# Performance work log

Measured on AMD Instinct MI355X. Metric: run time of the kernel, lower is better.

## Reference

```python
import jax, jax.numpy as jnp
import numpy as np

NH = 1024
NV = 31
LAYERS = 2
BS = 64
SEQ = 512
EPS = 1e-5


def _gru_layer(x_seq, h0, Wih, Whh, bih, bhh):
    """x_seq: [B,S,in], h0: [B,nh]. PyTorch GRU gate math. Returns [B,S,nh], h_last."""
    # Precompute input-side gates for all timesteps: [B,S,3nh]
    xg = jnp.einsum('bsi,gi->bsg', x_seq, Wih) + bih
    xg = jnp.swapaxes(xg, 0, 1)  # [S,B,3nh] for scan over time

    def step(h, xg_t):
        hg = h @ Whh.T + bhh  # [B,3nh]
        xr, xz, xn = jnp.split(xg_t, 3, axis=-1)
        hr, hz, hn = jnp.split(hg, 3, axis=-1)
        r = jax.nn.sigmoid(xr + hr)
        z = jax.nn.sigmoid(xz + hz)
        n = jnp.tanh(xn + r * hn)
        h_new = (1.0 - z) * n + z * h
        return h_new, h_new

    h_last, ys = jax.lax.scan(step, h0, xg)
    return jnp.swapaxes(ys, 0, 1), h_last  # [B,S,nh]


def setup_inputs() -> dict:
    key = jax.random.key(0)
    ks = jax.random.split(key, 16)
    s = 0.02
    inp = {
        'x': jax.random.randint(ks[0], (BS, SEQ), 0, NV),
        'h0': jnp.zeros((LAYERS, BS, NH), jnp.float32),
        'emb': jax.random.normal(ks[1], (NV, NH), jnp.float32) * s,
        'Wih0': jax.random.normal(ks[2], (3 * NH, NH), jnp.float32) * s,
        'Whh0': jax.random.normal(ks[3], (3 * NH, NH), jnp.float32) * s,
        'bih0': jnp.zeros((3 * NH,), jnp.float32),
        'bhh0': jnp.zeros((3 * NH,), jnp.float32),
        'Wih1': jax.random.normal(ks[4], (3 * NH, NH), jnp.float32) * s,
        'Whh1': jax.random.normal(ks[5], (3 * NH, NH), jnp.float32) * s,
        'bih1': jnp.zeros((3 * NH,), jnp.float32),
        'bhh1': jnp.zeros((3 * NH,), jnp.float32),
        'gamma': jnp.ones((NH,), jnp.float32),
        'beta': jnp.zeros((NH,), jnp.float32),
        'Wout': jax.random.normal(ks[6], (NV, NH), jnp.float32) * s,
        'bout': jnp.zeros((NV,), jnp.float32),
    }
    return inp


def reference(x, h0, emb, Wih0, Whh0, bih0, bhh0, Wih1, Whh1, bih1, bhh1,
              gamma, beta, Wout, bout):
    e = emb[x]  # [B,S,nh] embedding lookup
    y0, _ = _gru_layer(e, h0[0], Wih0, Whh0, bih0, bhh0)
    y1, _ = _gru_layer(y0, h0[1], Wih1, Whh1, bih1, bhh1)
    # BatchNorm1dFlat: flatten (B*S, nh), batch-statistics BN, reshape back
    flat = y1.reshape(-1, NH)
    mu = flat.mean(axis=0)
    var = flat.var(axis=0)  # biased, as in BN training
    bn = (y1 - mu) * jax.lax.rsqrt(var + EPS) * gamma + beta
    return bn @ Wout.T + bout  # [B,S,nv]
```

## Files before the change

### kernel.cpp

```cpp
#include <hip/hip_runtime.h>
#include <cstddef>
#include <stdint.h>

#define NHID 1024
#define NVOC 31
#define NB   64
#define NSEQ 512
#define NWRK 192
#define NGRID 256
#define NTHR 512
#define EPSV 1e-5f
#define RS2  36
#define SL   (NB*NHID)
#define XG_SLOTS 16

typedef __attribute__((ext_vector_type(8))) short short8;
typedef __attribute__((ext_vector_type(4))) float float4v;

#define OFF_F0  0
#define OFF_F1  4096
#define OFF_F2  8192
#define OFF_FIN 12288
#define CNT_BYTES 12352

#define M_OFF_Y0  12544
#define M_OFF_Y1  (M_OFF_Y0 + 513ull*SL*2)
#define M_OFF_H1I (M_OFF_Y1 + 512ull*SL*2)
#define M_OFF_T0  (M_OFF_H1I + (unsigned long long)SL*2)
#define M_OFF_ST  (M_OFF_T0 + 31ull*3*NHID*4)
#define M_OFF_XG  (M_OFF_ST + 16384ull)

#define LDS_BYTES 65024

__device__ __forceinline__ unsigned short f2bf(float f){
  unsigned u = __builtin_bit_cast(unsigned, f);
  u += 0x7fffu + ((u >> 16) & 1u);
  return (unsigned short)(u >> 16);
}
__device__ __forceinline__ float bf2f(unsigned short h){
  unsigned u = ((unsigned)h) << 16;
  return __builtin_bit_cast(float, u);
}
__device__ __forceinline__ float sigm(float x){ return 1.f/(1.f + __expf(-x)); }
__device__ __forceinline__ float tanh_f(float x){ return 1.f - 2.f/(__expf(2.f*x) + 1.f); }

__device__ __forceinline__ void burn(float& d){
#pragma unroll
  for (int i=0;i<16;++i)
    asm volatile("v_fmac_f32 %0, %1, %2" : "+v"(d) : "v"(d), "v"(d));
}

__device__ __forceinline__ void setflag(unsigned* f, unsigned v){
  __hip_atomic_store(f, v, __ATOMIC_RELAXED, __HIP_MEMORY_SCOPE_AGENT);
}
__device__ __forceinline__ void waitflags4(const unsigned* f, int base4, int target, int lane, float& d){
  const unsigned* p = f + (size_t)(base4 + (lane & 3))*16;
  for(;;){
    int v = (int)__hip_atomic_load(p, __ATOMIC_RELAXED, __HIP_MEMORY_SCOPE_AGENT);
    if (__all(v >= target)) break;
    burn(d);
  }
  asm volatile("" ::: "memory");
}
__device__ __forceinline__ void waitflag1(const unsigned* f, int idx, int target, float& d){
  const unsigned* p = f + (size_t)idx*16;
  while ((int)__hip_atomic_load(p, __ATOMIC_RELAXED, __HIP_MEMORY_SCOPE_AGENT) < target)
    burn(d);
  asm volatile("" ::: "memory");
}
__device__ __forceinline__ void waitflag1_slow(const unsigned* f, int idx, int target, float& d){
  const unsigned* p = f + (size_t)idx*16;
  while ((int)__hip_atomic_load(p, __ATOMIC_RELAXED, __HIP_MEMORY_SCOPE_AGENT) < target){
    burn(d); burn(d); burn(d); burn(d);
  }
  asm volatile("" ::: "memory");
}
__device__ __forceinline__ void sig(unsigned* c){
  __hip_atomic_fetch_add(c, 1u, __ATOMIC_RELAXED, __HIP_MEMORY_SCOPE_AGENT);
}
__device__ __forceinline__ void waitc(unsigned* c, unsigned v, float& d){
  while (__hip_atomic_load(c, __ATOMIC_RELAXED, __HIP_MEMORY_SCOPE_AGENT) < v)
    burn(d);
}

__device__ __forceinline__ void stc16(void* p, short8 v){
  asm volatile("global_store_dwordx4 %0, %1, off sc1"
               :: "v"((unsigned long long)(uintptr_t)p), "v"(v) : "memory");
}
__device__ __forceinline__ void stc4(void* p, float v){
  asm volatile("global_store_dword %0, %1, off sc1"
               :: "v"((unsigned long long)(uintptr_t)p), "v"(v) : "memory");
}
__device__ __forceinline__ void stc4u(void* p, unsigned v){
  asm volatile("global_store_dword %0, %1, off sc1"
               :: "v"((unsigned long long)(uintptr_t)p), "v"(v) : "memory");
}
__device__ __forceinline__ void drain_vm(){
  asm volatile("s_waitcnt vmcnt(0)" ::: "memory");
}

__device__ __forceinline__ void load_bfrags6(const float* W, int ch0,
                                             short8 (&bfr)[6][4], int lane, int wid)
{
  const int l15 = lane & 15, q = lane >> 4;
#pragma unroll
  for (int nt=0; nt<6; ++nt){
    int grow = (nt>>1)*NHID + ch0 + (nt&1)*16 + l15;
    const float* wp0 = W + (size_t)grow*NHID + wid*128 + q*8;
#pragma unroll
    for (int kt=0; kt<4; ++kt){
      const float* wp = wp0 + kt*32;
      short8 fr;
#pragma unroll
      for (int j=0;j<8;++j) fr[j] = (short)f2bf(wp[j]);
      bfr[nt][kt] = fr;
    }
  }
}
__device__ __forceinline__ void load_a2(const unsigned short* slab, int b0,
                                        short8 (&f)[2][4], int lane, int wid)
{
#pragma unroll
  for (int mt=0;mt<2;++mt){
    const short8* p = (const short8*)(slab + (size_t)(b0 + mt*16 + (lane&15))*NHID
                                      + wid*128 + (lane>>4)*8);
#pragma unroll
    for (int kt=0;kt<4;++kt) f[mt][kt] = p[kt*4];
  }
}
__device__ __forceinline__ void gemm2d(const short8 (&fA)[2][4],
                                       const short8 (&bfr)[6][4],
                                       float* red, int lane, int wid)
{
  const int l15 = lane & 15, q = lane >> 4;
  float4v acc[2][6];
#pragma unroll
  for (int mt=0; mt<2; ++mt)
#pragma unroll
    for (int nt=0; nt<6; ++nt) acc[mt][nt] = (float4v){0.f,0.f,0.f,0.f};
#pragma unroll
  for (int kt=0; kt<4; ++kt){
#pragma unroll
    for (int nt=0; nt<6; ++nt){
      acc[0][nt] = __builtin_amdgcn_mfma_f32_16x16x32_bf16(fA[0][kt], bfr[nt][kt], acc[0][nt],0,0,0);
      acc[1][nt] = __builtin_amdgcn_mfma_f32_16x16x32_bf16(fA[1][kt], bfr[nt][kt], acc[1][nt],0,0,0);
    }
  }
  if (wid >= 4){
#pragma unroll
    for (int mt=0; mt<2; ++mt)
#pragma unroll
      for (int nt=0; nt<6; ++nt){
        int n = nt*16 + l15, row = mt*16 + q*4;
        *(float4v*)(red + ((wid-4)*96 + n)*RS2 + row) = acc[mt][nt];
      }
  }
  __syncthreads();
  if (wid < 4){
#pragma unroll
    for (int mt=0; mt<2; ++mt)
#pragma unroll
      for (int nt=0; nt<6; ++nt){
        int n = nt*16 + l15, row = mt*16 + q*4;
        float4v* p = (float4v*)(red + (wid*96 + n)*RS2 + row);
        float4v v = *p;
        *p = v + acc[mt][nt];
      }
  }
  __syncthreads();
}

__global__ __launch_bounds__(NTHR, 2) void mgru_fused(
    const int*   __restrict__ x,    const float* __restrict__ h0,
    const float* __restrict__ emb,
    const float* __restrict__ Wih0, const float* __restrict__ Whh0,
    const float* __restrict__ bih0, const float* __restrict__ bhh0,
    const float* __restrict__ Wih1, const float* __restrict__ Whh1,
    const float* __restrict__ bih1, const float* __restrict__ bhh1,
    const float* __restrict__ gamma, const float* __restrict__ beta,
    const float* __restrict__ Wout, const float* __restrict__ bout,
    float* __restrict__ out, char* ws)
{
  __shared__ __align__(16) char smem[LDS_BYTES];
  float* red = (float*)smem;

  unsigned* f0  = (unsigned*)(ws + OFF_F0);
  unsigned* f1  = (unsigned*)(ws + OFF_F1);
  unsigned* f2  = (unsigned*)(ws + OFF_F2);
  unsigned* fin = (unsigned*)(ws + OFF_FIN);
  unsigned short* y0b   = (unsigned short*)(ws + M_OFF_Y0);
  unsigned short* y1    = (unsigned short*)(ws + M_OFF_Y1);
  unsigned short* h1i   = (unsigned short*)(ws + M_OFF_H1I);
  float*          T0    = (float*)(ws + M_OFF_T0);
  float*          stats = (float*)(ws + M_OFF_ST);
  float*          xgring= (float*)(ws + M_OFF_XG);

  const int tid  = threadIdx.x;
  const int lane = tid & 63;
  const int wid  = tid >> 6;
  const int wg   = blockIdx.x;
  const int l15 = lane & 15, q = lane >> 4;
  float dummy = (float)tid * 1e-30f + 1.0f;

  if (wg >= NWRK){
    for(;;){
      for (int i=0;i<64;++i) burn(dummy);
      unsigned v = __hip_atomic_load(fin, __ATOMIC_RELAXED, __HIP_MEMORY_SCOPE_AGENT);
      if (v >= (unsigned)NWRK) break;
    }
    if (tid == 0) __threadfence();
    __syncthreads();
    if (dummy == 1234.5678f) ((volatile float*)smem)[0] = dummy;
    goto epilogue;
  }

  {
    if (tid == 0) __threadfence();
    __syncthreads();

    const int role = (wg < 64) ? 0 : (wg < 128 ? 1 : 2);

    const int gm = tid >> 4;
    const int gc = (tid & 15) * 2;

    if (role == 0){
      const int rw = wg, bg = rw >> 5, cg = rw & 31;
      const int b0 = bg*32, ch0 = cg*32;
      const int fidx = bg*32 + cg;
      const int gbat = b0 + gm;
      short8 bfr0[6][4];
      float hprev[2];
      float br[2], bz[2], bn[2];

      {
        unsigned pk2 = 0;
#pragma unroll
        for (int j=0;j<2;++j){
          int ch = ch0 + gc + j;
          hprev[j] = h0[(size_t)gbat*NHID + ch];
          br[j] = bhh0[ch]; bz[j] = bhh0[NHID + ch]; bn[j] = bhh0[2*NHID + ch];
          pk2 |= (unsigned)f2bf(hprev[j]) << (16*j);
        }
        stc4u(y0b + (size_t)gbat*NHID + ch0 + gc, pk2);
        drain_vm();
      }
      __syncthreads();
      if (tid == 0) setflag(f0 + (size_t)fidx*16, 1u);

      for (int e = tid; e < NVOC*96; e += NTHR){
        int v = e / 96, n = e - v*96;
        int gate = n >> 5, c32 = n & 31;
        int grow = gate*NHID + ch0 + c32;
        const float4v* e4 = (const float4v*)(emb  + (size_t)v*NHID);
        const float4v* w4 = (const float4v*)(Wih0 + (size_t)grow*NHID);
        float acc = 0.f;
        for (int k=0;k<NHID/4;++k){
          float4v a = e4[k], bb = w4[k];
          acc += a[0]*bb[0] + a[1]*bb[1] + a[2]*bb[2] + a[3]*bb[3];
        }
        T0[(size_t)v*3*NHID + grow] = acc + bih0[grow];
      }
      load_bfrags6(Whh0, ch0, bfr0, lane, wid);
      __syncthreads();

      for (int t = 0; t < NSEQ; ++t){
        waitflags4(f0, bg*32 + wid*4, t+1, lane, dummy);
        short8 fA[2][4];
        load_a2(y0b + (size_t)t*SL, b0, fA, lane, wid);
        gemm2d(fA, bfr0, red, lane, wid);
        {
          int tok = x[(size_t)gbat*NSEQ + t];
          const float* tp = T0 + (size_t)tok*3*NHID;
          unsigned pk2 = 0;
#pragma unroll
          for (int j=0;j<2;++j){
            int c32 = gc + j, ch = ch0 + c32;
            float hr = br[j], hz = bz[j], hn = bn[j];
#pragma unroll
            for (int w=0;w<4;++w){
              hr += red[(w*96 +      c32)*RS2 + gm];
              hz += red[(w*96 + 32 + c32)*RS2 + gm];
              hn += red[(w*96 + 64 + c32)*RS2 + gm];
            }
            float r = sigm(tp[ch] + hr);
            float z = sigm(tp[NHID + ch] + hz);
            float n = tanh_f(tp[2*NHID + ch] + r*hn);
            float hnv = (1.f - z)*n + z*hprev[j];
            hprev[j] = hnv;
            pk2 |= (unsigned)f2bf(hnv) << (16*j);
          }
          stc4u(y0b + (size_t)(t+1)*SL + (size_t)gbat*NHID + ch0 + gc, pk2);
          drain_vm();
        }
        __syncthreads();
        if (tid == 0) setflag(f0 + (size_t)fidx*16, (unsigned)(t+2));
      }

    } else if (role == 1){
      const int rw = wg - 64, bg = rw >> 5, cg = rw & 31;
      const int b0 = bg*32, ch0 = cg*32;
      const int fidx = bg*32 + cg;
      short8 wf[6][4];
      load_bfrags6(Wih1, ch0, wf, lane, wid);
      __syncthreads();

      for (int t = 0; t < NSEQ; ++t){
        if ((t & 3) == 0 && t >= 16)
          waitflag1_slow(f2, fidx, t-11, dummy);
        waitflags4(f0, bg*32 + wid*4, t+2, lane, dummy);
        short8 fB[2][4];
        load_a2(y0b + (size_t)(t+1)*SL, b0, fB, lane, wid);
        gemm2d(fB, wf, red, lane, wid);
        float* xgw = xgring + ((size_t)(t & (XG_SLOTS-1))*64 + (size_t)fidx)*3072;
#pragma unroll
        for (int i=0;i<6;++i){
          int idx = tid + i*512;
          int n = idx >> 5, m = idx & 31;
          float v = bih1[(n>>5)*NHID + ch0 + (n&31)];
          v += red[(      n)*RS2 + m];
          v += red[( 96 + n)*RS2 + m];
          v += red[(192 + n)*RS2 + m];
          v += red[(288 + n)*RS2 + m];
          stc4(xgw + idx, v);
        }
        drain_vm();
        __syncthreads();
        if (tid == 0) setflag(f1 + (size_t)fidx*16, (unsigned)(t+2));
      }

    } else {
      const int rw = wg - 128, bg = rw >> 5, cg = rw & 31;
      const int b0 = bg*32, ch0 = cg*32;
      const int fidx = bg*32 + cg;
      const int gbat = b0 + gm;
      short8 bfrH[6][4];
      float hprev[2];
      float bhr[2], bhz[2], bhn[2];
      float s1[2] = {0,0}, s2[2] = {0,0};

      {
        unsigned pk2 = 0;
#pragma unroll
        for (int j=0;j<2;++j){
          int ch = ch0 + gc + j;
          hprev[j] = h0[(size_t)NB*NHID + (size_t)gbat*NHID + ch];
          bhr[j] = bhh1[ch]; bhz[j] = bhh1[NHID + ch]; bhn[j] = bhh1[2*NHID + ch];
          pk2 |= (unsigned)f2bf(hprev[j]) << (16*j);
        }
        stc4u(h1i + (size_t)gbat*NHID + ch0 + gc, pk2);
        drain_vm();
      }
      __syncthreads();
      if (tid == 0) setflag(f2 + (size_t)fidx*16, 1u);

      load_bfrags6(Whh1, ch0, bfrH, lane, wid);
      __syncthreads();

      for (int t = 0; t < NSEQ; ++t){
        waitflags4(f2, bg*32 + wid*4, t+1, lane, dummy);
        const unsigned short* hsrc = (t == 0) ? h1i : (y1 + (size_t)(t-1)*SL);
        short8 fH[2][4];
        load_a2(hsrc, b0, fH, lane, wid);
        gemm2d(fH, bfrH, red, lane, wid);
        {
          float hrv[2], hzv[2], hnv_[2];
#pragma unroll
          for (int j=0;j<2;++j){
            int c32 = gc + j;
            float hr = bhr[j], hz = bhz[j], hn = bhn[j];
#pragma unroll
            for (int w=0;w<4;++w){
              hr += red[(w*96 +      c32)*RS2 + gm];
              hz += red[(w*96 + 32 + c32)*RS2 + gm];
              hn += red[(w*96 + 64 + c32)*RS2 + gm];
            }
            hrv[j] = hr; hzv[j] = hz; hnv_[j] = hn;
          }
          waitflag1(f1, fidx, t+2, dummy);
          const float* xgt = xgring + ((size_t)(t & (XG_SLOTS-1))*64 + (size_t)fidx)*3072;
          unsigned pk2 = 0;
#pragma unroll
          for (int j=0;j<2;++j){
            int c32 = gc + j;
            float xr = __hip_atomic_load(xgt + (size_t)(     c32)*32 + gm, __ATOMIC_RELAXED, __HIP_MEMORY_SCOPE_AGENT);
            float xz = __hip_atomic_load(xgt + (size_t)(32 + c32)*32 + gm, __ATOMIC_RELAXED, __HIP_MEMORY_SCOPE_AGENT);
            float xn = __hip_atomic_load(xgt + (size_t)(64 + c32)*32 + gm, __ATOMIC_RELAXED, __HIP_MEMORY_SCOPE_AGENT);
            float r  = sigm(xr + hrv[j]);
            float z  = sigm(xz + hzv[j]);
            float nn = tanh_f(xn + r*hnv_[j]);
            float hnew = (1.f - z)*nn + z*hprev[j];
            hprev[j] = hnew;
            unsigned short hb = f2bf(hnew);
            pk2 |= (unsigned)hb << (16*j);
            float hq = bf2f(hb);
            s1[j] += hq; s2[j] += hq*hq;
          }
          stc4u(y1 + (size_t)t*SL + (size_t)gbat*NHID + ch0 + gc, pk2);
          drain_vm();
        }
        __syncthreads();
        if (tid == 0) setflag(f2 + (size_t)fidx*16, (unsigned)(t+2));
      }

      {
        float* sb = (float*)smem;
        __syncthreads();
#pragma unroll
        for (int j=0;j<2;++j) sb[(gc + j)*32 + gm] = s1[j];
        __syncthreads();
        if (tid < 32){
          float a = 0.f;
          for (int i=0;i<32;++i) a += sb[tid*32 + i];
          stats[(size_t)bg*2048 + ch0 + tid] = a;
        }
        __syncthreads();
#pragma unroll
        for (int j=0;j<2;++j) sb[(gc + j)*32 + gm] = s2[j];
        __syncthreads();
        if (tid < 32){
          float a = 0.f;
          for (int i=0;i<32;++i) a += sb[tid*32 + i];
          stats[(size_t)bg*2048 + 1024 + ch0 + tid] = a;
        }
      }
    }

    __syncthreads();
    if (tid == 0){
      __threadfence();
      sig(fin);
      waitc(fin, NWRK, dummy);
      __threadfence();
    }
    __syncthreads();
    if (dummy == 1234.5678f) ((volatile float*)smem)[0] = dummy;
  }

epilogue:
  {
    const float inv_n = 1.f/32768.f;

    float* bpart    = (float*)smem;
    float* bprime_l = (float*)(smem + 2048);
    {
      int v = tid >> 4, k0 = tid & 15;
      float partial = 0.f;
      if (v < NVOC){
        for (int k = k0; k < NHID; k += 16){
          float s1k = stats[k] + stats[2048 + k];
          float s2k = stats[1024 + k] + stats[3072 + k];
          float mu  = s1k*inv_n;
          float var = s2k*inv_n - mu*mu;
          float sc  = gamma[k]*rsqrtf(var + EPSV);
          partial += (beta[k] - mu*sc) * Wout[(size_t)v*NHID + k];
        }
      }
      bpart[tid] = partial;
    }
    __syncthreads();
    if (tid < 32){
      float bpv = 0.f;
      for (int j=0;j<16;++j) bpv += bpart[tid*16 + j];
      bprime_l[tid] = (tid < NVOC) ? (bpv + bout[tid]) : 0.f;
    }
    __syncthreads();
    float bp_a = bprime_l[l15];
    float bp_b = (l15 < 15) ? bprime_l[16 + l15] : 0.f;
    __syncthreads();

    unsigned short* wsc = (unsigned short*)smem;
    for (int e = tid; e < NVOC*1032; e += NTHR){
      int v = e / 1032, k = e - v*1032;
      float val = 0.f;
      if (k < NHID){
        float s1k = stats[k] + stats[2048 + k];
        float s2k = stats[1024 + k] + stats[3072 + k];
        float mu  = s1k*inv_n;
        float var = s2k*inv_n - mu*mu;
        float sc  = gamma[k]*rsqrtf(var + EPSV);
        val = Wout[(size_t)v*NHID + k] * sc;
      }
      wsc[e] = f2bf(val);
    }
    __syncthreads();

    unsigned short* y1b = (unsigned short*)(ws + M_OFF_Y1);
    int wglob = wg*8 + wid;
    if ((wglob & 3) == 0){
      int J = wglob >> 2;
      float4v acc[4][2];
#pragma unroll
      for (int mt=0;mt<4;++mt){ acc[mt][0] = (float4v){0,0,0,0}; acc[mt][1] = (float4v){0,0,0,0}; }
      const unsigned short* abase = y1b + (size_t)(J*64 + l15)*NHID + q*8;
      const short8 zero8 = (short8){0,0,0,0,0,0,0,0};
#pragma unroll 4
      for (int kt=0; kt<32; ++kt){
        short8 bv0 = *(const short8*)(wsc + (size_t)l15*1032 + kt*32 + q*8);
        short8 bv1 = (l15 < 15) ? *(const short8*)(wsc + (size_t)(16+l15)*1032 + kt*32 + q*8) : zero8;
        short8 a0 = *(const short8*)(abase + (size_t)kt*32);
        short8 a1 = *(const short8*)(abase + 16*NHID + (size_t)kt*32);
        short8 a2 = *(const short8*)(abase + 32*NHID + (size_t)kt*32);
        short8 a3 = *(const short8*)(abase + 48*NHID + (size_t)kt*32);
        acc[0][0] = __builtin_amdgcn_mfma_f32_16x16x32_bf16(a0, bv0, acc[0][0],0,0,0);
        acc[1][0] = __builtin_amdgcn_mfma_f32_16x16x32_bf16(a1, bv0, acc[1][0],0,0,0);
        acc[2][0] = __builtin_amdgcn_mfma_f32_16x16x32_bf16(a2, bv0, acc[2][0],0,0,0);
        acc[3][0] = __builtin_amdgcn_mfma_f32_16x16x32_bf16(a3, bv0, acc[3][0],0,0,0);
        acc[0][1] = __builtin_amdgcn_mfma_f32_16x16x32_bf16(a0, bv1, acc[0][1],0,0,0);
        acc[1][1] = __builtin_amdgcn_mfma_f32_16x16x32_bf16(a1, bv1, acc[1][1],0,0,0);
        acc[2][1] = __builtin_amdgcn_mfma_f32_16x16x32_bf16(a2, bv1, acc[2][1],0,0,0);
        acc[3][1] = __builtin_amdgcn_mfma_f32_16x16x32_bf16(a3, bv1, acc[3][1],0,0,0);
      }
#pragma unroll
      for (int mt=0;mt<4;++mt){
#pragma unroll
        for (int nt=0;nt<2;++nt){
          int v = nt*16 + l15;
          if (v < NVOC){
            float bpv = (nt==0) ? bp_a : bp_b;
            int r0 = J*64 + mt*16 + q*4;
#pragma unroll
            for (int i2=0;i2<4;++i2){
              int r = r0 + i2;
              int bb = r & 63, tt = r >> 6;
              out[(size_t)(bb*NSEQ + tt)*NVOC + v] = acc[mt][nt][i2] + bpv;
            }
          }
        }
      }
    }
  }
}

extern "C" void kernel_launch(void* const* d_in, const int* in_sizes, int n_in,
                              void* d_out, int out_size, void* d_ws, size_t ws_size,
                              hipStream_t stream) {
  (void)in_sizes; (void)n_in; (void)out_size; (void)ws_size;
  hipMemsetAsync(d_ws, 0, CNT_BYTES, stream);
  mgru_fused<<<dim3(NGRID), dim3(NTHR), 0, stream>>>(
      (const int*)d_in[0],  (const float*)d_in[1],  (const float*)d_in[2],
      (const float*)d_in[3], (const float*)d_in[4], (const float*)d_in[5],
      (const float*)d_in[6], (const float*)d_in[7], (const float*)d_in[8],
      (const float*)d_in[9], (const float*)d_in[10], (const float*)d_in[11],
      (const float*)d_in[12], (const float*)d_in[13], (const float*)d_in[14],
      (float*)d_out, (char*)d_ws);
}
```

Measured before the change: 3.785 ms.

## Remap gate threads for conflict-free LDS reads, stage stores, prefetch layer-1 input gates

The gate-math threads now use a batch-fastest mapping, so reads of the reduction buffer in LDS and of the xg ring run along contiguous rows. Results go through a small LDS staging buffer and are then written out with the original coalesced per-row global layout. Layer 1 also tries to load its input-gate values before the GEMM when the producer flag is already set, to hide that latency. The cost is one extra __syncthreads and an LDS round trip on every timestep.

```diff
diff --git a/kernel.cpp b/kernel.cpp
--- a/kernel.cpp
+++ b/kernel.cpp
@@ -30,6 +30,7 @@
 #define M_OFF_ST  (M_OFF_T0 + 31ull*3*NHID*4)
 #define M_OFF_XG  (M_OFF_ST + 16384ull)
 
+#define STG_OFF   55296
 #define LDS_BYTES 65024
 
 __device__ __forceinline__ unsigned short f2bf(float f){
@@ -83,10 +84,6 @@
     burn(d);
 }
 
-__device__ __forceinline__ void stc16(void* p, short8 v){
-  asm volatile("global_store_dwordx4 %0, %1, off sc1"
-               :: "v"((unsigned long long)(uintptr_t)p), "v"(v) : "memory");
-}
 __device__ __forceinline__ void stc4(void* p, float v){
   asm volatile("global_store_dword %0, %1, off sc1"
                :: "v"((unsigned long long)(uintptr_t)p), "v"(v) : "memory");
@@ -183,6 +180,7 @@
 {
   __shared__ __align__(16) char smem[LDS_BYTES];
   float* red = (float*)smem;
+  unsigned* stg = (unsigned*)(smem + STG_OFF);
 
   unsigned* f0  = (unsigned*)(ws + OFF_F0);
   unsigned* f1  = (unsigned*)(ws + OFF_F1);
@@ -220,14 +218,17 @@
 
     const int role = (wg < 64) ? 0 : (wg < 128 ? 1 : 2);
 
-    const int gm = tid >> 4;
-    const int gc = (tid & 15) * 2;
+    const int gmA = tid & 31;
+    const int gcA = (tid >> 5) * 2;
+    const int gmB = tid >> 4;
+    const int gcB = (tid & 15) * 2;
 
     if (role == 0){
       const int rw = wg, bg = rw >> 5, cg = rw & 31;
       const int b0 = bg*32, ch0 = cg*32;
       const int fidx = bg*32 + cg;
-      const int gbat = b0 + gm;
+      const int gbatA = b0 + gmA;
+      const int gbatB = b0 + gmB;
       short8 bfr0[6][4];
       float hprev[2];
       float br[2], bz[2], bn[2];
@@ -236,12 +237,12 @@
         unsigned pk2 = 0;
 #pragma unroll
         for (int j=0;j<2;++j){
-          int ch = ch0 + gc + j;
-          hprev[j] = h0[(size_t)gbat*NHID + ch];
+          int ch = ch0 + gcA + j;
+          hprev[j] = h0[(size_t)gbatA*NHID + ch];
           br[j] = bhh0[ch]; bz[j] = bhh0[NHID + ch]; bn[j] = bhh0[2*NHID + ch];
           pk2 |= (unsigned)f2bf(hprev[j]) << (16*j);
         }
-        stc4u(y0b + (size_t)gbat*NHID + ch0 + gc, pk2);
+        stc4u(y0b + (size_t)gbatA*NHID + ch0 + gcA, pk2);
         drain_vm();
       }
       __syncthreads();
@@ -269,18 +270,18 @@
         load_a2(y0b + (size_t)t*SL, b0, fA, lane, wid);
         gemm2d(fA, bfr0, red, lane, wid);
         {
-          int tok = x[(size_t)gbat*NSEQ + t];
+          int tok = x[(size_t)gbatA*NSEQ + t];
           const float* tp = T0 + (size_t)tok*3*NHID;
           unsigned pk2 = 0;
 #pragma unroll
           for (int j=0;j<2;++j){
-            int c32 = gc + j, ch = ch0 + c32;
+            int c32 = gcA + j, ch = ch0 + c32;
             float hr = br[j], hz = bz[j], hn = bn[j];
 #pragma unroll
             for (int w=0;w<4;++w){
-              hr += red[(w*96 +      c32)*RS2 + gm];
-              hz += red[(w*96 + 32 + c32)*RS2 + gm];
-              hn += red[(w*96 + 64 + c32)*RS2 + gm];
+              hr += red[(w*96 +      c32)*RS2 + gmA];
+              hz += red[(w*96 + 32 + c32)*RS2 + gmA];
+              hn += red[(w*96 + 64 + c32)*RS2 + gmA];
             }
             float r = sigm(tp[ch] + hr);
             float z = sigm(tp[NHID + ch] + hz);
@@ -289,7 +290,12 @@
             hprev[j] = hnv;
             pk2 |= (unsigned)f2bf(hnv) << (16*j);
           }
-          stc4u(y0b + (size_t)(t+1)*SL + (size_t)gbat*NHID + ch0 + gc, pk2);
+          stg[gmA*17 + (gcA>>1)] = pk2;
+        }
+        __syncthreads();
+        {
+          unsigned v = stg[gmB*17 + (gcB>>1)];
+          stc4u(y0b + (size_t)(t+1)*SL + (size_t)gbatB*NHID + ch0 + gcB, v);
           drain_vm();
         }
         __syncthreads();
@@ -332,7 +338,8 @@
       const int rw = wg - 128, bg = rw >> 5, cg = rw & 31;
       const int b0 = bg*32, ch0 = cg*32;
       const int fidx = bg*32 + cg;
-      const int gbat = b0 + gm;
+      const int gbatA = b0 + gmA;
+      const int gbatB = b0 + gmB;
       short8 bfrH[6][4];
       float hprev[2];
       float bhr[2], bhz[2], bhn[2];
@@ -342,12 +349,12 @@
         unsigned pk2 = 0;
 #pragma unroll
         for (int j=0;j<2;++j){
-          int ch = ch0 + gc + j;
-          hprev[j] = h0[(size_t)NB*NHID + (size_t)gbat*NHID + ch];
+          int ch = ch0 + gcA + j;
+          hprev[j] = h0[(size_t)NB*NHID + (size_t)gbatA*NHID + ch];
           bhr[j] = bhh1[ch]; bhz[j] = bhh1[NHID + ch]; bhn[j] = bhh1[2*NHID + ch];
           pk2 |= (unsigned)f2bf(hprev[j]) << (16*j);
         }
-        stc4u(h1i + (size_t)gbat*NHID + ch0 + gc, pk2);
+        stc4u(h1i + (size_t)gbatA*NHID + ch0 + gcA, pk2);
         drain_vm();
       }
       __syncthreads();
@@ -361,33 +368,48 @@
         const unsigned short* hsrc = (t == 0) ? h1i : (y1 + (size_t)(t-1)*SL);
         short8 fH[2][4];
         load_a2(hsrc, b0, fH, lane, wid);
+
+        const float* xgt = xgring + ((size_t)(t & (XG_SLOTS-1))*64 + (size_t)fidx)*3072;
+        float xr[2], xz[2], xn[2];
+        unsigned fv = __hip_atomic_load(f1 + (size_t)fidx*16, __ATOMIC_RELAXED, __HIP_MEMORY_SCOPE_AGENT);
+        bool early = __all((int)fv >= t+2);
+        if (early){
+#pragma unroll
+          for (int j=0;j<2;++j){
+            int c32 = gcA + j;
+            xr[j] = __hip_atomic_load(xgt + (size_t)(     c32)*32 + gmA, __ATOMIC_RELAXED, __HIP_MEMORY_SCOPE_AGENT);
+            xz[j] = __hip_atomic_load(xgt + (size_t)(32 + c32)*32 + gmA, __ATOMIC_RELAXED, __HIP_MEMORY_SCOPE_AGENT);
+            xn[j] = __hip_atomic_load(xgt + (size_t)(64 + c32)*32 + gmA, __ATOMIC_RELAXED, __HIP_MEMORY_SCOPE_AGENT);
+          }
+        }
+
         gemm2d(fH, bfrH, red, lane, wid);
+
         {
-          float hrv[2], hzv[2], hnv_[2];
+          if (!early){
+            waitflag1(f1, fidx, t+2, dummy);
+#pragma unroll
+            for (int j=0;j<2;++j){
+              int c32 = gcA + j;
+              xr[j] = __hip_atomic_load(xgt + (size_t)(     c32)*32 + gmA, __ATOMIC_RELAXED, __HIP_MEMORY_SCOPE_AGENT);
+              xz[j] = __hip_atomic_load(xgt + (size_t)(32 + c32)*32 + gmA, __ATOMIC_RELAXED, __HIP_MEMORY_SCOPE_AGENT);
+              xn[j] = __hip_atomic_load(xgt + (size_t)(64 + c32)*32 + gmA, __ATOMIC_RELAXED, __HIP_MEMORY_SCOPE_AGENT);
+            }
+          }
+          unsigned pk2 = 0;
 #pragma unroll
           for (int j=0;j<2;++j){
-            int c32 = gc + j;
+            int c32 = gcA + j;
             float hr = bhr[j], hz = bhz[j], hn = bhn[j];
 #pragma unroll
             for (int w=0;w<4;++w){
-              hr += red[(w*96 +      c32)*RS2 + gm];
-              hz += red[(w*96 + 32 + c32)*RS2 + gm];
-              hn += red[(w*96 + 64 + c32)*RS2 + gm];
+              hr += red[(w*96 +      c32)*RS2 + gmA];
+              hz += red[(w*96 + 32 + c32)*RS2 + gmA];
+              hn += red[(w*96 + 64 + c32)*RS2 + gmA];
             }
-            hrv[j] = hr; hzv[j] = hz; hnv_[j] = hn;
-          }
-          waitflag1(f1, fidx, t+2, dummy);
-          const float* xgt = xgring + ((size_t)(t & (XG_SLOTS-1))*64 + (size_t)fidx)*3072;
-          unsigned pk2 = 0;
-#pragma unroll
-          for (int j=0;j<2;++j){
-            int c32 = gc + j;
-            float xr = __hip_atomic_load(xgt + (size_t)(     c32)*32 + gm, __ATOMIC_RELAXED, __HIP_MEMORY_SCOPE_AGENT);
-            float xz = __hip_atomic_load(xgt + (size_t)(32 + c32)*32 + gm, __ATOMIC_RELAXED, __HIP_MEMORY_SCOPE_AGENT);
-            float xn = __hip_atomic_load(xgt + (size_t)(64 + c32)*32 + gm, __ATOMIC_RELAXED, __HIP_MEMORY_SCOPE_AGENT);
-            float r  = sigm(xr + hrv[j]);
-            float z  = sigm(xz + hzv[j]);
-            float nn = tanh_f(xn + r*hnv_[j]);
+            float r  = sigm(xr[j] + hr);
+            float z  = sigm(xz[j] + hz);
+            float nn = tanh_f(xn[j] + r*hn);
             float hnew = (1.f - z)*nn + z*hprev[j];
             hprev[j] = hnew;
             unsigned short hb = f2bf(hnew);
@@ -395,7 +417,12 @@
             float hq = bf2f(hb);
             s1[j] += hq; s2[j] += hq*hq;
           }
-          stc4u(y1 + (size_t)t*SL + (size_t)gbat*NHID + ch0 + gc, pk2);
+          stg[gmA*17 + (gcA>>1)] = pk2;
+        }
+        __syncthreads();
+        {
+          unsigned v = stg[gmB*17 + (gcB>>1)];
+          stc4u(y1 + (size_t)t*SL + (size_t)gbatB*NHID + ch0 + gcB, v);
           drain_vm();
         }
         __syncthreads();
@@ -406,7 +433,7 @@
         float* sb = (float*)smem;
         __syncthreads();
 #pragma unroll
-        for (int j=0;j<2;++j) sb[(gc + j)*32 + gm] = s1[j];
+        for (int j=0;j<2;++j) sb[(gcA + j)*32 + gmA] = s1[j];
         __syncthreads();
         if (tid < 32){
           float a = 0.f;
@@ -415,7 +442,7 @@
         }
         __syncthreads();
 #pragma unroll
-        for (int j=0;j<2;++j) sb[(gc + j)*32 + gm] = s2[j];
+        for (int j=0;j<2;++j) sb[(gcA + j)*32 + gmA] = s2[j];
         __syncthreads();
         if (tid < 32){
           float a = 0.f;
```

After: 3.524 ms. 6.9% less time.
